# Kernel optimization log

Hardware: AMD Instinct MI355X
Metric: run time of the kernel (lower is better)

## Reference

```python
import jax, jax.numpy as jnp
import numpy as np

DIM = 768
HEADS = 12
HEAD_DIM = DIM // HEADS
SEQ = 196
BATCH = 64
SCALE = HEAD_DIM ** -0.5


def setup_inputs() -> dict:
    key = jax.random.key(0)
    ks = jax.random.split(key, 5)
    x = jax.random.normal(ks[0], (BATCH, SEQ, DIM), dtype=jnp.float32)
    W_qkv = jax.random.normal(ks[1], (DIM, 3 * DIM), dtype=jnp.float32) * (DIM ** -0.5)
    static_a = jax.random.truncated_normal(ks[2], -2.0, 2.0, (1, HEADS, SEQ, SEQ), dtype=jnp.float32)
    W_proj = jax.random.normal(ks[3], (DIM, DIM), dtype=jnp.float32) * (DIM ** -0.5)
    b_proj = jnp.zeros((DIM,), dtype=jnp.float32)
    return {"x": x, "W_qkv": W_qkv, "static_a": static_a, "W_proj": W_proj, "b_proj": b_proj}


def reference(x, W_qkv, static_a, W_proj, b_proj):
    B, N, C = x.shape
    qkv = (x @ W_qkv).reshape(B, N, 3, HEADS, HEAD_DIM)
    qkv = jnp.transpose(qkv, (2, 0, 3, 1, 4))  # [3, B, H, N, D]
    q, k, v = qkv[0], qkv[1], qkv[2]
    attn = jnp.einsum('bhnd,bhmd->bhnm', q, k) * SCALE
    attn = jax.nn.softmax(attn, axis=-1) + static_a  # post-softmax additive bias
    out = jnp.einsum('bhnm,bhmd->bhnd', attn, v)  # [B, H, N, D]
    out = jnp.transpose(out, (0, 2, 1, 3)).reshape(B, N, C)
    return out @ W_proj + b_proj
```

## Files before the change

### kernel.cpp

```cpp
#include <hip/hip_runtime.h>
#include <stdint.h>

#define DIM 768
#define HEADS 12
#define SEQ 196
#define BATCH 64
#define NTOK (BATCH*SEQ)
#define QKVLD (3*DIM)
#define SCALE 0.125f

using short8  = __attribute__((ext_vector_type(8))) short;
using short4v = __attribute__((ext_vector_type(4))) short;
using float4v = __attribute__((ext_vector_type(4))) float;
using ushort4v = __attribute__((ext_vector_type(4))) unsigned short;

static __device__ __forceinline__ unsigned short f2bf(float f) {
  union { float f; unsigned u; } v; v.f = f;
  unsigned u = v.u;
  u += 0x7fffu + ((u >> 16) & 1u);
  return (unsigned short)(u >> 16);
}

#if defined(__has_builtin)
#if __has_builtin(__builtin_amdgcn_global_load_lds)
#define HAS_GLL 1
#endif
#endif

static __device__ __forceinline__ void gll16(const unsigned short* g, unsigned short* l) {
#ifdef HAS_GLL
  __builtin_amdgcn_global_load_lds(
      (const __attribute__((address_space(1))) void*)g,
      (__attribute__((address_space(3))) void*)l, 16, 0, 0);
#else
  const int lane = threadIdx.x & 63;
  *(short8*)(l + lane * 8) = *(const short8*)g;
#endif
}

__global__ __launch_bounds__(256) void cast_x_kernel(const float* __restrict__ in,
                                                     unsigned short* __restrict__ out) {
  int i = blockIdx.x * 256 + threadIdx.x;
  float4 v = ((const float4*)in)[i];
  ushort4v o;
  o.x = f2bf(v.x); o.y = f2bf(v.y); o.z = f2bf(v.z); o.w = f2bf(v.w);
  ((ushort4v*)out)[i] = o;
}

__global__ __launch_bounds__(256) void transpose_cast_kernel(const float* __restrict__ in,
                                                             unsigned short* __restrict__ out,
                                                             int R, int C) {
  __shared__ float tile[32][33];
  int c0 = blockIdx.x * 32, r0 = blockIdx.y * 32;
  int tx = threadIdx.x, ty = threadIdx.y;
  for (int i = 0; i < 32; i += 8)
    tile[ty + i][tx] = in[(size_t)(r0 + ty + i) * C + c0 + tx];
  __syncthreads();
  for (int i = 0; i < 32; i += 8)
    out[(size_t)(c0 + ty + i) * R + r0 + tx] = f2bf(tile[tx][ty + i]);
}

template <int MODE>
__global__ __launch_bounds__(256) void gemm_kernel(const unsigned short* __restrict__ A,
                                                   const unsigned short* __restrict__ Bt,
                                                   const float* __restrict__ bias,
                                                   unsigned short* __restrict__ outB,
                                                   float* __restrict__ outF) {
  constexpr int K = 768;
  __shared__ __align__(16) unsigned short Als[128 * 32];
  __shared__ __align__(16) unsigned short Bls[128 * 32];
  const int tid = threadIdx.x;
  const int wid = tid >> 6, lane = tid & 63;
  const int s = lane & 15, q = lane >> 4;
  const int wr = wid >> 1, wc = wid & 1;

  const int nbx = gridDim.x;
  const int nb = gridDim.x * gridDim.y;
  int id = blockIdx.y * nbx + blockIdx.x;
  {
    int x = id & 7, lid = id >> 3;
    int per = nb >> 3, big = nb & 7;
    id = (x < big) ? x * (per + 1) + lid
                   : big * (per + 1) + (x - big) * per + lid;
  }
  const int m0 = (id / nbx) * 128;
  const int n0 = (id % nbx) * 128;

  float4v acc[4][4];
  for (int i = 0; i < 4; i++)
    for (int j = 0; j < 4; j++) acc[i][j] = (float4v){0.f, 0.f, 0.f, 0.f};

  const int srow = lane >> 2;
  const int scol = (lane & 3) * 8;

  const unsigned short* ga = A  + (size_t)(m0 + wid * 32 + srow) * K + scol;
  const unsigned short* gb = Bt + (size_t)(n0 + wid * 32 + srow) * K + scol;
  unsigned short* la = &Als[wid * 32 * 32];
  unsigned short* lb = &Bls[wid * 32 * 32];

  for (int kt = 0; kt < K; kt += 32) {
    gll16(ga,           la);
    gll16(ga + 16 * K,  la + 16 * 32);
    gll16(gb,           lb);
    gll16(gb + 16 * K,  lb + 16 * 32);
    ga += 32; gb += 32;
    __syncthreads();

    short8 af[4], bf[4];
    for (int i = 0; i < 4; i++)
      af[i] = *(const short8*)&Als[(wr * 64 + i * 16 + s) * 32 + q * 8];
    for (int j = 0; j < 4; j++)
      bf[j] = *(const short8*)&Bls[(wc * 64 + j * 16 + s) * 32 + q * 8];
    for (int i = 0; i < 4; i++)
      for (int j = 0; j < 4; j++) {
        if (MODE == 0)
          acc[i][j] = __builtin_amdgcn_mfma_f32_16x16x32_bf16(bf[j], af[i], acc[i][j], 0, 0, 0);
        else
          acc[i][j] = __builtin_amdgcn_mfma_f32_16x16x32_bf16(af[i], bf[j], acc[i][j], 0, 0, 0);
      }
    __syncthreads();
  }

  if (MODE == 0) {
    for (int i = 0; i < 4; i++) {
      size_t mrow = (size_t)(m0 + wr * 64 + i * 16 + s) * QKVLD;
      for (int j = 0; j < 4; j++) {
        int n = n0 + wc * 64 + j * 16 + q * 4;
        ushort4v ov;
        ov.x = f2bf(acc[i][j][0]); ov.y = f2bf(acc[i][j][1]);
        ov.z = f2bf(acc[i][j][2]); ov.w = f2bf(acc[i][j][3]);
        *(ushort4v*)&outB[mrow + n] = ov;
      }
    }
  } else {
    for (int i = 0; i < 4; i++) {
      int mbase = m0 + wr * 64 + i * 16 + q * 4;
      for (int j = 0; j < 4; j++) {
        int ng = n0 + wc * 64 + j * 16 + s;
        float bv = bias[ng];
        for (int r = 0; r < 4; r++)
          outF[(size_t)(mbase + r) * 768 + ng] = acc[i][j][r] + bv;
      }
    }
  }
}

__global__ __launch_bounds__(256) void attn_kernel(const unsigned short* __restrict__ qkv,
                                                   const float* __restrict__ static_a,
                                                   unsigned short* __restrict__ outA) {
  constexpr int WV = 228;
  __shared__ __align__(16) unsigned short Vt[64 * WV];
  const int tid = threadIdx.x, wid = tid >> 6, lane = tid & 63;
  const int s = lane & 15, q = lane >> 4;
  const int bh = blockIdx.x;
  const int b = bh / 12, h = bh % 12;
  const unsigned short* Qb = qkv + (size_t)b * SEQ * QKVLD + h * 64;
  const unsigned short* Kb = Qb + 768;
  const unsigned short* Vb = Qb + 1536;

  {
    const int ms = tid & 63;
    const int d0 = (tid >> 6) * 16;
    for (int mb = 0; mb < 4; ++mb) {
      int m = mb * 64 + ms;
      if (m < 224) {
        if (m < 196) {
          short8 v0 = *(const short8*)&Vb[(size_t)m * QKVLD + d0];
          short8 v1 = *(const short8*)&Vb[(size_t)m * QKVLD + d0 + 8];
          for (int j = 0; j < 8; j++) Vt[(d0 + j) * WV + m] = (unsigned short)v0[j];
          for (int j = 0; j < 8; j++) Vt[(d0 + 8 + j) * WV + m] = (unsigned short)v1[j];
        } else {
          for (int j = 0; j < 16; j++) Vt[(d0 + j) * WV + m] = 0;
        }
      }
    }
  }
  __syncthreads();

  const int pmbase = (s >> 2) * 8 + (s & 3);

  for (int qt = wid; qt < 13; qt += 4) {
    const int n0 = qt * 16;
    const int nq = n0 + s;
    const int nql = nq > 195 ? 195 : nq;
    short8 qf0 = *(const short8*)&Qb[(size_t)nql * QKVLD + q * 8];
    short8 qf1 = *(const short8*)&Qb[(size_t)nql * QKVLD + 32 + q * 8];

    float4v sacc[14];
    for (int tt = 0; tt < 13; tt++) {
      int t = tt >> 1, h4 = tt & 1;
      int m = t * 32 + h4 * 4 + pmbase;
      if (m > 195) m = 195;
      short8 kf0 = *(const short8*)&Kb[(size_t)m * QKVLD + q * 8];
      short8 kf1 = *(const short8*)&Kb[(size_t)m * QKVLD + 32 + q * 8];
      float4v z = (float4v){0.f, 0.f, 0.f, 0.f};
      z = __builtin_amdgcn_mfma_f32_16x16x32_bf16(kf0, qf0, z, 0, 0, 0);
      z = __builtin_amdgcn_mfma_f32_16x16x32_bf16(kf1, qf1, z, 0, 0, 0);
      sacc[tt] = z;
    }
    sacc[13] = (float4v){0.f, 0.f, 0.f, 0.f};

    float mx = -3.0e38f;
    for (int tt = 0; tt < 12; tt++)
      for (int i = 0; i < 4; i++) mx = fmaxf(mx, sacc[tt][i]);
    if (q == 0)
      for (int i = 0; i < 4; i++) mx = fmaxf(mx, sacc[12][i]);
    mx = fmaxf(mx, __shfl_xor(mx, 16));
    mx = fmaxf(mx, __shfl_xor(mx, 32));
    const float CE = SCALE * 1.44269504f;
    float sm = 0.f;
    for (int tt = 0; tt < 12; tt++)
      for (int i = 0; i < 4; i++) {
        float e = __builtin_amdgcn_exp2f((sacc[tt][i] - mx) * CE);
        sacc[tt][i] = e; sm += e;
      }
    if (q == 0) {
      for (int i = 0; i < 4; i++) {
        float e = __builtin_amdgcn_exp2f((sacc[12][i] - mx) * CE);
        sacc[12][i] = e; sm += e;
      }
    } else {
      sacc[12] = (float4v){0.f, 0.f, 0.f, 0.f};
    }
    sm += __shfl_xor(sm, 16);
    sm += __shfl_xor(sm, 32);
    const float inv = 1.0f / sm;

    const float* sa = static_a + ((size_t)h * SEQ + nql) * SEQ;
    short8 pfrag[7];
    for (int t = 0; t < 7; t++) {
      short8 pf;
      for (int h4 = 0; h4 < 2; h4++) {
        int tt = 2 * t + h4;
        bool valid = (tt < 12) || (tt == 12 && q == 0);
        float4v a4 = (float4v){0.f, 0.f, 0.f, 0.f};
        if (valid) a4 = *(const float4v*)(sa + t * 32 + q * 8 + h4 * 4);
        int src = valid ? tt : 13;
        for (int i = 0; i < 4; i++) {
          float pv = valid ? (sacc[src][i] * inv + a4[i]) : 0.f;
          pf[h4 * 4 + i] = (short)f2bf(pv);
        }
      }
      pfrag[t] = pf;
    }

    for (int dt = 0; dt < 4; dt++) {
      float4v o = (float4v){0.f, 0.f, 0.f, 0.f};
      for (int t = 0; t < 7; t++) {
        const unsigned short* vp = &Vt[(dt * 16 + s) * WV + t * 32 + q * 8];
        short4v v0 = *(const short4v*)vp;
        short4v v1 = *(const short4v*)(vp + 4);
        short8 vf;
        vf[0] = v0[0]; vf[1] = v0[1]; vf[2] = v0[2]; vf[3] = v0[3];
        vf[4] = v1[0]; vf[5] = v1[1]; vf[6] = v1[2]; vf[7] = v1[3];
        o = __builtin_amdgcn_mfma_f32_16x16x32_bf16(vf, pfrag[t], o, 0, 0, 0);
      }
      if (nq < 196) {
        ushort4v ov;
        ov.x = f2bf(o[0]); ov.y = f2bf(o[1]); ov.z = f2bf(o[2]); ov.w = f2bf(o[3]);
        *(ushort4v*)&outA[((size_t)b * SEQ + nq) * DIM + h * 64 + dt * 16 + q * 4] = ov;
      }
    }
  }
}

extern "C" void kernel_launch(void* const* d_in, const int* in_sizes, int n_in,
                              void* d_out, int out_size, void* d_ws, size_t ws_size,
                              hipStream_t stream) {
  const float* x        = (const float*)d_in[0];
  const float* Wqkv     = (const float*)d_in[1];
  const float* static_a = (const float*)d_in[2];
  const float* Wproj    = (const float*)d_in[3];
  const float* bproj    = (const float*)d_in[4];
  float* out = (float*)d_out;

  unsigned char* ws = (unsigned char*)d_ws;
  size_t off = 0;
  unsigned short* qkv_ws = (unsigned short*)(ws + off); off += (size_t)NTOK * QKVLD * 2;
  unsigned short* xa_ws  = (unsigned short*)(ws + off); off += (size_t)NTOK * DIM * 2;
  unsigned short* wqkvt  = (unsigned short*)(ws + off); off += (size_t)3 * DIM * DIM * 2;
  unsigned short* wprojt = (unsigned short*)(ws + off); off += (size_t)DIM * DIM * 2;

  cast_x_kernel<<<NTOK * DIM / 4 / 256, 256, 0, stream>>>(x, xa_ws);
  transpose_cast_kernel<<<dim3(3 * DIM / 32, DIM / 32), dim3(32, 8), 0, stream>>>(Wqkv, wqkvt, DIM, 3 * DIM);
  transpose_cast_kernel<<<dim3(DIM / 32, DIM / 32), dim3(32, 8), 0, stream>>>(Wproj, wprojt, DIM, DIM);
  gemm_kernel<0><<<dim3(3 * DIM / 128, NTOK / 128), 256, 0, stream>>>(xa_ws, wqkvt, nullptr, qkv_ws, nullptr);
  attn_kernel<<<BATCH * HEADS, 256, 0, stream>>>(qkv_ws, static_a, xa_ws);
  gemm_kernel<1><<<dim3(DIM / 128, NTOK / 128), 256, 0, stream>>>(xa_ws, wprojt, bproj, nullptr, out);
}
```

Before: 249.0 us.

## Load 64-wide K chunks per barrier, drop block swizzle, vectorize proj epilogue

The GEMM main loop now stages two 32-wide K slices into separate LDS buffers per iteration, which halves the number of barrier pairs and puts more loads in flight per sync. The XCD-aware block-id remapping is removed in favour of plain blockIdx tiling. The MODE 1 path now uses the same transposed MFMA operand order as MODE 0, so each lane writes 4 consecutive floats with a float4 bias load and store instead of strided scalar stores. This doubles LDS use per block and may reduce L2 locality across XCDs.

```diff
diff --git a/kernel.cpp b/kernel.cpp
--- a/kernel.cpp
+++ b/kernel.cpp
@@ -67,24 +67,14 @@
                                                    unsigned short* __restrict__ outB,
                                                    float* __restrict__ outF) {
   constexpr int K = 768;
-  __shared__ __align__(16) unsigned short Als[128 * 32];
-  __shared__ __align__(16) unsigned short Bls[128 * 32];
+  __shared__ __align__(16) unsigned short Als[2][128 * 32];
+  __shared__ __align__(16) unsigned short Bls[2][128 * 32];
   const int tid = threadIdx.x;
   const int wid = tid >> 6, lane = tid & 63;
   const int s = lane & 15, q = lane >> 4;
   const int wr = wid >> 1, wc = wid & 1;
-
-  const int nbx = gridDim.x;
-  const int nb = gridDim.x * gridDim.y;
-  int id = blockIdx.y * nbx + blockIdx.x;
-  {
-    int x = id & 7, lid = id >> 3;
-    int per = nb >> 3, big = nb & 7;
-    id = (x < big) ? x * (per + 1) + lid
-                   : big * (per + 1) + (x - big) * per + lid;
-  }
-  const int m0 = (id / nbx) * 128;
-  const int n0 = (id % nbx) * 128;
+  const int m0 = blockIdx.y * 128;
+  const int n0 = blockIdx.x * 128;
 
   float4v acc[4][4];
   for (int i = 0; i < 4; i++)
@@ -95,29 +85,33 @@
 
   const unsigned short* ga = A  + (size_t)(m0 + wid * 32 + srow) * K + scol;
   const unsigned short* gb = Bt + (size_t)(n0 + wid * 32 + srow) * K + scol;
-  unsigned short* la = &Als[wid * 32 * 32];
-  unsigned short* lb = &Bls[wid * 32 * 32];
-
-  for (int kt = 0; kt < K; kt += 32) {
-    gll16(ga,           la);
-    gll16(ga + 16 * K,  la + 16 * 32);
-    gll16(gb,           lb);
-    gll16(gb + 16 * K,  lb + 16 * 32);
-    ga += 32; gb += 32;
+  unsigned short* la0 = &Als[0][wid * 32 * 32];
+  unsigned short* la1 = &Als[1][wid * 32 * 32];
+  unsigned short* lb0 = &Bls[0][wid * 32 * 32];
+  unsigned short* lb1 = &Bls[1][wid * 32 * 32];
+
+  for (int kt = 0; kt < K; kt += 64) {
+    gll16(ga,                la0);
+    gll16(ga + 16 * K,       la0 + 16 * 32);
+    gll16(ga + 32,           la1);
+    gll16(ga + 32 + 16 * K,  la1 + 16 * 32);
+    gll16(gb,                lb0);
+    gll16(gb + 16 * K,       lb0 + 16 * 32);
+    gll16(gb + 32,           lb1);
+    gll16(gb + 32 + 16 * K,  lb1 + 16 * 32);
+    ga += 64; gb += 64;
     __syncthreads();
 
-    short8 af[4], bf[4];
-    for (int i = 0; i < 4; i++)
-      af[i] = *(const short8*)&Als[(wr * 64 + i * 16 + s) * 32 + q * 8];
-    for (int j = 0; j < 4; j++)
-      bf[j] = *(const short8*)&Bls[(wc * 64 + j * 16 + s) * 32 + q * 8];
-    for (int i = 0; i < 4; i++)
-      for (int j = 0; j < 4; j++) {
-        if (MODE == 0)
-          acc[i][j] = __builtin_amdgcn_mfma_f32_16x16x32_bf16(bf[j], af[i], acc[i][j], 0, 0, 0);
-        else
-          acc[i][j] = __builtin_amdgcn_mfma_f32_16x16x32_bf16(af[i], bf[j], acc[i][j], 0, 0, 0);
-      }
+    for (int hh = 0; hh < 2; hh++) {
+      short8 af[4], bfr[4];
+      for (int i = 0; i < 4; i++)
+        af[i] = *(const short8*)&Als[hh][(wr * 64 + i * 16 + s) * 32 + q * 8];
+      for (int j = 0; j < 4; j++)
+        bfr[j] = *(const short8*)&Bls[hh][(wc * 64 + j * 16 + s) * 32 + q * 8];
+      for (int i = 0; i < 4; i++)
+        for (int j = 0; j < 4; j++)
+          acc[i][j] = __builtin_amdgcn_mfma_f32_16x16x32_bf16(bfr[j], af[i], acc[i][j], 0, 0, 0);
+    }
     __syncthreads();
   }
 
@@ -134,12 +128,13 @@
     }
   } else {
     for (int i = 0; i < 4; i++) {
-      int mbase = m0 + wr * 64 + i * 16 + q * 4;
+      size_t mrow = (size_t)(m0 + wr * 64 + i * 16 + s) * 768;
       for (int j = 0; j < 4; j++) {
-        int ng = n0 + wc * 64 + j * 16 + s;
-        float bv = bias[ng];
-        for (int r = 0; r < 4; r++)
-          outF[(size_t)(mbase + r) * 768 + ng] = acc[i][j][r] + bv;
+        int n = n0 + wc * 64 + j * 16 + q * 4;
+        float4v bv = *(const float4v*)&bias[n];
+        float4v o;
+        for (int r = 0; r < 4; r++) o[r] = acc[i][j][r] + bv[r];
+        *(float4v*)&outF[mrow + n] = o;
       }
     }
   }
```

Result: slower. 263.8 us (+6.0%).
